# Kernel optimization log

Measured on AMD Instinct MI355X. Metric: run time of the kernel, lower is better.

Reference implementation:

```python
import jax, jax.numpy as jnp
import numpy as np

EPS = 1e-05


def setup_inputs() -> dict:
    key = jax.random.key(0)
    k1, k2, k3, k4 = jax.random.split(key, 4)
    B, N, L, J = 1, 256, 192, 32
    n_feat_out = 128
    d2 = J * J  # 1024
    x_down = jax.random.normal(k1, (B, N, L, J), dtype=jnp.float32)
    x_down_w = jax.random.normal(k2, (B, N, L, J), dtype=jnp.float32)
    a_2 = jnp.ones((d2,), dtype=jnp.float32)
    b_2 = jnp.zeros((d2,), dtype=jnp.float32)
    # nn.Linear default init: U(-1/sqrt(fan_in), 1/sqrt(fan_in))
    bound = 1.0 / np.sqrt(d2)
    W = jax.random.uniform(k3, (d2, n_feat_out), dtype=jnp.float32, minval=-bound, maxval=bound)
    b = jax.random.uniform(k4, (n_feat_out,), dtype=jnp.float32, minval=-bound, maxval=bound)
    return {"x_down": x_down, "x_down_w": x_down_w, "a_2": a_2, "b_2": b_2, "W": W, "b": b}


def reference(x_down, x_down_w, a_2, b_2, W, b):
    B, N, L, J = x_down.shape
    # outer-product contraction over MSA dim: (B,L,L,J,J)
    pair = jnp.einsum('bnij,bnlm->biljm', x_down, x_down_w)
    pair = pair.reshape(B, L, L, J * J)
    # LayerNorm over last dim (biased variance, matching torch unbiased=False)
    mean = pair.mean(axis=-1, keepdims=True)
    var = pair.var(axis=-1, keepdims=True)
    pair = a_2 * (pair - mean) / jnp.sqrt(var + EPS) + b_2
    # Linear projection J^2 -> n_feat_out
    return pair @ W + b
```

## Files before the change

### kernel.cpp

```cpp
#include <hip/hip_runtime.h>
#include <hip/hip_bf16.h>
#include <stdint.h>

#define NN   256
#define LL   192
#define MDIM 6144
#define D2   1024
#define FF   128

typedef __bf16 bf16x8 __attribute__((ext_vector_type(8)));
typedef float  f32x4  __attribute__((ext_vector_type(4)));

#define MFMA16(a, b, c) __builtin_amdgcn_mfma_f32_16x16x32_bf16(a, b, c, 0, 0, 0)

__device__ __forceinline__ void gload_lds16(const void* g, void* l) {
  __builtin_amdgcn_global_load_lds(
      (__attribute__((address_space(1))) void*)(g),
      (__attribute__((address_space(3))) void*)(l),
      16, 0, 0);
}

static __device__ __forceinline__ unsigned short bf16_bits(float v) {
  __bf16 h = (__bf16)v;
  return __builtin_bit_cast(unsigned short, h);
}

__global__ __launch_bounds__(256)
void prep_all(const float* __restrict__ x1, const float* __restrict__ x2,
              const float* __restrict__ W, const float* __restrict__ a2,
              const float* __restrict__ b2, const float* __restrict__ bias,
              __bf16* __restrict__ At, __bf16* __restrict__ Bt,
              __bf16* __restrict__ WB, float* __restrict__ S,
              float* __restrict__ T) {
  __shared__ float tile[32][33];
  const int b = blockIdx.x;
  const int t = threadIdx.x;
  if (b < 3072) {
    const float* src = (b < 1536) ? x1 : x2;
    __bf16* dst = (b < 1536) ? At : Bt;
    const int bb = (b < 1536) ? b : b - 1536;
    const int m0 = (bb % 192) * 32;
    const int k0 = (bb / 192) * 32;
    {
      const int kr = t >> 3, mc = (t & 7) * 4;
      const float4 v = *(const float4*)&src[(size_t)(k0 + kr) * MDIM + m0 + mc];
      tile[kr][mc + 0] = v.x;
      tile[kr][mc + 1] = v.y;
      tile[kr][mc + 2] = v.z;
      tile[kr][mc + 3] = v.w;
    }
    __syncthreads();
    {
      const int mr = t >> 3, kc = (t & 7) * 4;
      ushort4 u;
      u.x = bf16_bits(tile[kc + 0][mr]);
      u.y = bf16_bits(tile[kc + 1][mr]);
      u.z = bf16_bits(tile[kc + 2][mr]);
      u.w = bf16_bits(tile[kc + 3][mr]);
      *(ushort4*)&dst[(size_t)(m0 + mr) * NN + k0 + kc] = u;
    }
  } else {
    const int f = b - 3072;
    float s = 0.f, tt = 0.f;
#pragma unroll
    for (int it = 0; it < 4; ++it) {
      const int k = t + it * 256;
      const float wv = W[(size_t)k * FF + f];
      const __bf16 wa = (__bf16)(a2[k] * wv);
      WB[(size_t)(k >> 5) * 4096 + f * 32 + ((k >> 3) & 3) * 8 + (k & 7)] = wa;
      s += (float)wa;
      tt += b2[k] * wv;
    }
#pragma unroll
    for (int off = 32; off; off >>= 1) {
      s += __shfl_xor(s, off);
      tt += __shfl_xor(tt, off);
    }
    const int wv_ = t >> 6, ln = t & 63;
    if (ln == 0) { tile[0][wv_] = s; tile[1][wv_] = tt; }
    __syncthreads();
    if (t == 0) {
      S[f] = tile[0][0] + tile[0][1] + tile[0][2] + tile[0][3];
      T[f] = tile[1][0] + tile[1][1] + tile[1][2] + tile[1][3] + bias[f];
    }
  }
}

__global__ __launch_bounds__(512, 4)
void fused10(const __bf16* __restrict__ At, const __bf16* __restrict__ Bt,
             const __bf16* __restrict__ WB, const float* __restrict__ S,
             const float* __restrict__ T, float* __restrict__ out) {
  __shared__ uint8_t lds[65536];
  __shared__ float mean_s[32], rstd_s[32];

  const int tid = threadIdx.x;
  const int w = tid >> 6;
  const int lane = tid & 63;
  const int q = lane >> 4;
  const int c = lane & 15;

  const int b = blockIdx.x;
  const int xcd = b & 7;
  const int s_ = b >> 3;
  const int bx = (xcd >> 1) * 12 + (s_ % 12);
  const int by = (xcd & 1) * 12 + (s_ / 12);
  const int m0 = bx * 128, n0 = by * 256;

  uint8_t* As = lds;
  uint8_t* Bs = lds + 16384;

  const int l8 = lane & 7;
  const int r8 = lane >> 3;
  const int gsw = l8 ^ r8;

  f32x4 acc[4][4];
#pragma unroll
  for (int i = 0; i < 4; ++i)
#pragma unroll
    for (int j = 0; j < 4; ++j)
      acc[i][j] = (f32x4){0.f, 0.f, 0.f, 0.f};

  const int mbase = (w & 1) * 64;
  const int nbase = (w >> 1) * 64;

  {
    const __bf16* gA = At + (size_t)(m0 + w * 16 + r8) * NN + gsw * 8;
    const __bf16* gB = Bt + (size_t)(n0 + w * 32 + r8) * NN + gsw * 8;
#pragma unroll 1
    for (int kb = 0; kb < 4; ++kb) {
      __syncthreads();
#pragma unroll
      for (int j = 0; j < 2; ++j)
        gload_lds16(gA + (size_t)j * 8 * NN, As + (w * 16 + j * 8) * 128);
#pragma unroll
      for (int j = 0; j < 4; ++j)
        gload_lds16(gB + (size_t)j * 8 * NN, Bs + (w * 32 + j * 8) * 128);
      __syncthreads();
#pragma unroll
      for (int ks = 0; ks < 2; ++ks) {
        const int slot = ((ks * 4 + q) ^ (lane & 7)) * 16;
        bf16x8 a[4];
#pragma unroll
        for (int t4 = 0; t4 < 4; ++t4)
          a[t4] = *(const bf16x8*)(As + (mbase + t4 * 16 + c) * 128 + slot);
#pragma unroll
        for (int tj = 0; tj < 4; ++tj) {
          const bf16x8 bfr =
              *(const bf16x8*)(Bs + (nbase + tj * 16 + c) * 128 + slot);
#pragma unroll
          for (int ti = 0; ti < 4; ++ti)
            acc[ti][tj] = MFMA16(a[ti], bfr, acc[ti][tj]);
        }
      }
      gA += 64;
      gB += 64;
    }
  }

  const int fs = w * 16;
  const __bf16* wbp = WB + (fs + c) * 32 + q * 8;
  bf16x8 pb[8];
  pb[0] = *(const bf16x8*)(wbp);
  pb[1] = *(const bf16x8*)(wbp + 4096);

  __syncthreads();

  const int i_hi = w & 1, l_hi = w >> 1;
#pragma unroll
  for (int ab = 0; ab < 2; ++ab) {
#pragma unroll
    for (int cb = 0; cb < 2; ++cb) {
      float s1 = 0.f, s2 = 0.f;
#pragma unroll
      for (int dti = 0; dti < 2; ++dti)
#pragma unroll
        for (int dtj = 0; dtj < 2; ++dtj)
#pragma unroll
          for (int reg = 0; reg < 4; ++reg) {
            const float v = acc[ab * 2 + dti][cb * 2 + dtj][reg];
            s1 += v; s2 += v * v;
          }
#pragma unroll
      for (int off = 32; off; off >>= 1) {
        s1 += __shfl_xor(s1, off);
        s2 += __shfl_xor(s2, off);
      }
      const float mean = s1 * (1.0f / 1024.0f);
      const float var = s2 * (1.0f / 1024.0f) - mean * mean;
      const float rstd = rsqrtf(var + 1e-5f);
      const int r = (i_hi * 2 + ab) * 8 + l_hi * 2 + cb;
      if (lane == 0) { mean_s[r] = mean; rstd_s[r] = rstd; }
      const int r7 = r & 7;
#pragma unroll
      for (int dti = 0; dti < 2; ++dti)
#pragma unroll
        for (int dtj = 0; dtj < 2; ++dtj)
#pragma unroll
          for (int rp = 0; rp < 4; rp += 2) {
            const float x = acc[ab * 2 + dti][cb * 2 + dtj][rp];
            const float y = acc[ab * 2 + dti][cb * 2 + dtj][rp + 1];
            const float send = (c & 1) ? x : y;
            const float recv = __shfl_xor(send, 1);
            const float vlo = (c & 1) ? recv : x;
            const float vhi = (c & 1) ? y : recv;
            const int reg_w = (c & 1) ? rp + 1 : rp;
            const int j = dti * 16 + q * 4 + reg_w;
            const int mm0 = dtj * 16 + (c & ~1);
            const int k = j * 32 + mm0;
            const int g = k >> 3;
            const int G = g ^ (g >> 4) ^ r7;
            const uint32_t dw =
                ((uint32_t)bf16_bits(vhi) << 16) | (uint32_t)bf16_bits(vlo);
            *(uint32_t*)(lds + r * 2048 + G * 16 + (mm0 & 7) * 2) = dw;
          }
    }
  }

  __syncthreads();
  __builtin_amdgcn_sched_barrier(0);

#pragma unroll
  for (int p = 2; p < 8; ++p)
    pb[p] = *(const bf16x8*)(wbp + p * 4096);

  f32x4 acc2[2];
  acc2[0] = (f32x4){0.f, 0.f, 0.f, 0.f};
  acc2[1] = (f32x4){0.f, 0.f, 0.f, 0.f};
  const int c7 = c & 7;
#pragma unroll
  for (int kstep = 0; kstep < 32; ++kstep) {
    const int g = kstep * 4 + q;
    const int G = g ^ (g >> 4) ^ c7;
    const bf16x8 a0 = *(const bf16x8*)(lds + c * 2048 + G * 16);
    const bf16x8 a1 = *(const bf16x8*)(lds + (16 + c) * 2048 + G * 16);
    acc2[0] = MFMA16(a0, pb[kstep & 7], acc2[0]);
    acc2[1] = MFMA16(a1, pb[kstep & 7], acc2[1]);
    if (kstep < 24)
      pb[kstep & 7] = *(const bf16x8*)(wbp + (kstep + 8) * 4096);
  }

  const float S0 = S[fs + c], T0 = T[fs + c];
#pragma unroll
  for (int reg = 0; reg < 4; ++reg) {
    const int r0 = q * 4 + reg;
    const int r1 = 16 + r0;
    {
      const float mean = mean_s[r0], rstd = rstd_s[r0];
      const int i = bx * 4 + (r0 >> 3);
      const int l = by * 8 + (r0 & 7);
      out[((size_t)i * LL + l) * FF + fs + c] =
          rstd * (acc2[0][reg] - mean * S0) + T0;
    }
    {
      const float mean = mean_s[r1], rstd = rstd_s[r1];
      const int i = bx * 4 + (r1 >> 3);
      const int l = by * 8 + (r1 & 7);
      out[((size_t)i * LL + l) * FF + fs + c] =
          rstd * (acc2[1][reg] - mean * S0) + T0;
    }
  }
}

extern "C" void kernel_launch(void* const* d_in, const int* in_sizes, int n_in,
                              void* d_out, int out_size, void* d_ws, size_t ws_size,
                              hipStream_t stream) {
  const float* x_down   = (const float*)d_in[0];
  const float* x_down_w = (const float*)d_in[1];
  const float* a2       = (const float*)d_in[2];
  const float* b2       = (const float*)d_in[3];
  const float* W        = (const float*)d_in[4];
  const float* bias     = (const float*)d_in[5];
  float* out = (float*)d_out;

  uint8_t* ws = (uint8_t*)d_ws;
  __bf16* At  = (__bf16*)(ws);
  __bf16* Bt  = (__bf16*)(ws + 3145728);
  __bf16* WB  = (__bf16*)(ws + 6291456);
  float*  S   = (float*)(ws + 6553600);
  float*  T   = (float*)(ws + 6554112);

  prep_all<<<dim3(3200), dim3(256), 0, stream>>>(x_down, x_down_w, W, a2, b2,
                                                 bias, At, Bt, WB, S, T);
  fused10<<<dim3(1152), dim3(512), 0, stream>>>(At, Bt, WB, S, T, out);
}
```

Before: 124.9 us.

## Double-buffer LDS loads and enlarge tiles to 256x256 with 1024-thread blocks

Doubles the M tile per block (256x256 output tile, 16 waves) and double-buffers the A/B LDS tiles so the next K-slice's global-to-LDS loads overlap the current MFMA work, using explicit vmcnt waits. The grid is halved to 576 blocks, with 128 KB of dynamic LDS and the XCD-aware block mapping adjusted to match. Only 8 of the 16 waves run the second projection GEMM, each now handling 64 rows. The large LDS footprint limits residency to one block per CU, and idle waves in the epilogue may reduce utilisation.

```diff
diff --git a/kernel.cpp b/kernel.cpp
--- a/kernel.cpp
+++ b/kernel.cpp
@@ -86,12 +86,12 @@
   }
 }
 
-__global__ __launch_bounds__(512, 4)
-void fused10(const __bf16* __restrict__ At, const __bf16* __restrict__ Bt,
+__global__ __launch_bounds__(1024, 4)
+void fused11(const __bf16* __restrict__ At, const __bf16* __restrict__ Bt,
              const __bf16* __restrict__ WB, const float* __restrict__ S,
              const float* __restrict__ T, float* __restrict__ out) {
-  __shared__ uint8_t lds[65536];
-  __shared__ float mean_s[32], rstd_s[32];
+  extern __shared__ uint8_t lds[];
+  __shared__ float mean_s[64], rstd_s[64];
 
   const int tid = threadIdx.x;
   const int w = tid >> 6;
@@ -102,12 +102,14 @@
   const int b = blockIdx.x;
   const int xcd = b & 7;
   const int s_ = b >> 3;
-  const int bx = (xcd >> 1) * 12 + (s_ % 12);
-  const int by = (xcd & 1) * 12 + (s_ / 12);
-  const int m0 = bx * 128, n0 = by * 256;
-
-  uint8_t* As = lds;
-  uint8_t* Bs = lds + 16384;
+  const int bx = (xcd >> 1) * 6 + (s_ % 6);
+  const int by = (xcd & 1) * 12 + (s_ / 6);
+  const int m0 = bx * 256, n0 = by * 256;
+
+  uint8_t* As0 = lds;
+  uint8_t* Bs0 = lds + 32768;
+  uint8_t* As1 = lds + 65536;
+  uint8_t* Bs1 = lds + 98304;
 
   const int l8 = lane & 7;
   const int r8 = lane >> 3;
@@ -120,52 +122,69 @@
     for (int j = 0; j < 4; ++j)
       acc[i][j] = (f32x4){0.f, 0.f, 0.f, 0.f};
 
-  const int mbase = (w & 1) * 64;
-  const int nbase = (w >> 1) * 64;
-
-  {
-    const __bf16* gA = At + (size_t)(m0 + w * 16 + r8) * NN + gsw * 8;
-    const __bf16* gB = Bt + (size_t)(n0 + w * 32 + r8) * NN + gsw * 8;
-#pragma unroll 1
-    for (int kb = 0; kb < 4; ++kb) {
-      __syncthreads();
+  const int mbase = (w & 3) * 64;
+  const int nbase = (w >> 2) * 64;
+
+  const __bf16* gA = At + (size_t)(m0 + w * 16 + r8) * NN + gsw * 8;
+  const __bf16* gB = Bt + (size_t)(n0 + w * 16 + r8) * NN + gsw * 8;
+
+#pragma unroll
+  for (int j = 0; j < 2; ++j)
+    gload_lds16(gA + (size_t)j * 8 * NN, As0 + (w * 16 + j * 8) * 128);
+#pragma unroll
+  for (int j = 0; j < 2; ++j)
+    gload_lds16(gB + (size_t)j * 8 * NN, Bs0 + (w * 16 + j * 8) * 128);
+
+#pragma unroll
+  for (int kb = 0; kb < 4; ++kb) {
+    uint8_t* Ac = (kb & 1) ? As1 : As0;
+    uint8_t* Bc = (kb & 1) ? Bs1 : Bs0;
+    if (kb < 3) {
+      uint8_t* An = (kb & 1) ? As0 : As1;
+      uint8_t* Bn = (kb & 1) ? Bs0 : Bs1;
+      const __bf16* ga = gA + (size_t)(kb + 1) * 64;
+      const __bf16* gb = gB + (size_t)(kb + 1) * 64;
 #pragma unroll
       for (int j = 0; j < 2; ++j)
-        gload_lds16(gA + (size_t)j * 8 * NN, As + (w * 16 + j * 8) * 128);
-#pragma unroll
-      for (int j = 0; j < 4; ++j)
-        gload_lds16(gB + (size_t)j * 8 * NN, Bs + (w * 32 + j * 8) * 128);
-      __syncthreads();
-#pragma unroll
-      for (int ks = 0; ks < 2; ++ks) {
-        const int slot = ((ks * 4 + q) ^ (lane & 7)) * 16;
-        bf16x8 a[4];
-#pragma unroll
-        for (int t4 = 0; t4 < 4; ++t4)
-          a[t4] = *(const bf16x8*)(As + (mbase + t4 * 16 + c) * 128 + slot);
-#pragma unroll
-        for (int tj = 0; tj < 4; ++tj) {
-          const bf16x8 bfr =
-              *(const bf16x8*)(Bs + (nbase + tj * 16 + c) * 128 + slot);
-#pragma unroll
-          for (int ti = 0; ti < 4; ++ti)
-            acc[ti][tj] = MFMA16(a[ti], bfr, acc[ti][tj]);
-        }
+        gload_lds16(ga + (size_t)j * 8 * NN, An + (w * 16 + j * 8) * 128);
+#pragma unroll
+      for (int j = 0; j < 2; ++j)
+        gload_lds16(gb + (size_t)j * 8 * NN, Bn + (w * 16 + j * 8) * 128);
+      asm volatile("s_waitcnt vmcnt(4)" ::: "memory");
+    } else {
+      asm volatile("s_waitcnt vmcnt(0)" ::: "memory");
+    }
+    __builtin_amdgcn_s_barrier();
+    __builtin_amdgcn_sched_barrier(0);
+#pragma unroll
+    for (int ks = 0; ks < 2; ++ks) {
+      const int slot = ((ks * 4 + q) ^ l8) * 16;
+      bf16x8 a[4];
+#pragma unroll
+      for (int t4 = 0; t4 < 4; ++t4)
+        a[t4] = *(const bf16x8*)(Ac + (mbase + t4 * 16 + c) * 128 + slot);
+#pragma unroll
+      for (int tj = 0; tj < 4; ++tj) {
+        const bf16x8 bfr =
+            *(const bf16x8*)(Bc + (nbase + tj * 16 + c) * 128 + slot);
+#pragma unroll
+        for (int ti = 0; ti < 4; ++ti)
+          acc[ti][tj] = MFMA16(a[ti], bfr, acc[ti][tj]);
       }
-      gA += 64;
-      gB += 64;
-    }
+    }
+    asm volatile("s_waitcnt lgkmcnt(0)" ::: "memory");
+    __builtin_amdgcn_s_barrier();
   }
 
   const int fs = w * 16;
   const __bf16* wbp = WB + (fs + c) * 32 + q * 8;
   bf16x8 pb[8];
-  pb[0] = *(const bf16x8*)(wbp);
-  pb[1] = *(const bf16x8*)(wbp + 4096);
-
-  __syncthreads();
-
-  const int i_hi = w & 1, l_hi = w >> 1;
+  if (w < 8) {
+    pb[0] = *(const bf16x8*)(wbp);
+    pb[1] = *(const bf16x8*)(wbp + 4096);
+  }
+
+  const int i_hi = w & 3, l_hi = w >> 2;
 #pragma unroll
   for (int ab = 0; ab < 2; ++ab) {
 #pragma unroll
@@ -217,47 +236,45 @@
   }
 
   __syncthreads();
-  __builtin_amdgcn_sched_barrier(0);
-
-#pragma unroll
-  for (int p = 2; p < 8; ++p)
-    pb[p] = *(const bf16x8*)(wbp + p * 4096);
-
-  f32x4 acc2[2];
-  acc2[0] = (f32x4){0.f, 0.f, 0.f, 0.f};
-  acc2[1] = (f32x4){0.f, 0.f, 0.f, 0.f};
-  const int c7 = c & 7;
-#pragma unroll
-  for (int kstep = 0; kstep < 32; ++kstep) {
-    const int g = kstep * 4 + q;
-    const int G = g ^ (g >> 4) ^ c7;
-    const bf16x8 a0 = *(const bf16x8*)(lds + c * 2048 + G * 16);
-    const bf16x8 a1 = *(const bf16x8*)(lds + (16 + c) * 2048 + G * 16);
-    acc2[0] = MFMA16(a0, pb[kstep & 7], acc2[0]);
-    acc2[1] = MFMA16(a1, pb[kstep & 7], acc2[1]);
-    if (kstep < 24)
-      pb[kstep & 7] = *(const bf16x8*)(wbp + (kstep + 8) * 4096);
-  }
-
-  const float S0 = S[fs + c], T0 = T[fs + c];
-#pragma unroll
-  for (int reg = 0; reg < 4; ++reg) {
-    const int r0 = q * 4 + reg;
-    const int r1 = 16 + r0;
-    {
-      const float mean = mean_s[r0], rstd = rstd_s[r0];
-      const int i = bx * 4 + (r0 >> 3);
-      const int l = by * 8 + (r0 & 7);
-      out[((size_t)i * LL + l) * FF + fs + c] =
-          rstd * (acc2[0][reg] - mean * S0) + T0;
-    }
-    {
-      const float mean = mean_s[r1], rstd = rstd_s[r1];
-      const int i = bx * 4 + (r1 >> 3);
-      const int l = by * 8 + (r1 & 7);
-      out[((size_t)i * LL + l) * FF + fs + c] =
-          rstd * (acc2[1][reg] - mean * S0) + T0;
-    }
+
+  if (w < 8) {
+    __builtin_amdgcn_sched_barrier(0);
+#pragma unroll
+    for (int p = 2; p < 8; ++p)
+      pb[p] = *(const bf16x8*)(wbp + p * 4096);
+
+    f32x4 acc2[4];
+#pragma unroll
+    for (int rr = 0; rr < 4; ++rr) acc2[rr] = (f32x4){0.f, 0.f, 0.f, 0.f};
+    const int c7 = c & 7;
+#pragma unroll
+    for (int kstep = 0; kstep < 32; ++kstep) {
+      const int g = kstep * 4 + q;
+      const int G = g ^ (g >> 4) ^ c7;
+      const bf16x8 a0 = *(const bf16x8*)(lds + (size_t)(c)      * 2048 + G * 16);
+      const bf16x8 a1 = *(const bf16x8*)(lds + (size_t)(16 + c) * 2048 + G * 16);
+      const bf16x8 a2 = *(const bf16x8*)(lds + (size_t)(32 + c) * 2048 + G * 16);
+      const bf16x8 a3 = *(const bf16x8*)(lds + (size_t)(48 + c) * 2048 + G * 16);
+      acc2[0] = MFMA16(a0, pb[kstep & 7], acc2[0]);
+      acc2[1] = MFMA16(a1, pb[kstep & 7], acc2[1]);
+      acc2[2] = MFMA16(a2, pb[kstep & 7], acc2[2]);
+      acc2[3] = MFMA16(a3, pb[kstep & 7], acc2[3]);
+      if (kstep < 24)
+        pb[kstep & 7] = *(const bf16x8*)(wbp + (kstep + 8) * 4096);
+    }
+
+    const float S0 = S[fs + c], T0 = T[fs + c];
+#pragma unroll
+    for (int rr = 0; rr < 4; ++rr)
+#pragma unroll
+      for (int reg = 0; reg < 4; ++reg) {
+        const int r = rr * 16 + q * 4 + reg;
+        const float mean = mean_s[r], rstd = rstd_s[r];
+        const int i = bx * 8 + (r >> 3);
+        const int l = by * 8 + (r & 7);
+        out[((size_t)i * LL + l) * FF + fs + c] =
+            rstd * (acc2[rr][reg] - mean * S0) + T0;
+      }
   }
 }
 
@@ -279,7 +296,10 @@
   float*  S   = (float*)(ws + 6553600);
   float*  T   = (float*)(ws + 6554112);
 
+  hipFuncSetAttribute((const void*)fused11,
+                      hipFuncAttributeMaxDynamicSharedMemorySize, 131072);
+
   prep_all<<<dim3(3200), dim3(256), 0, stream>>>(x_down, x_down_w, W, a2, b2,
                                                  bias, At, Bt, WB, S, T);
-  fused10<<<dim3(1152), dim3(512), 0, stream>>>(At, Bt, WB, S, T, out);
-}
+  fused11<<<dim3(576), dim3(1024), 131072, stream>>>(At, Bt, WB, S, T, out);
+}
```

New measurement: 128.6 us. +3.0%, slower.

## Double-buffer LDS K-tiles with async global loads to overlap GEMM loads and MFMA

Applied to the files above, without the earlier changes.

Replaces the single-buffered 64-wide K loop (4 iterations, two full syncthreads each) with a double-buffered 32-wide K loop (8 iterations). The next tile is prefetched into the alternate LDS buffer via global_load_lds, with explicit vmcnt waits and raw s_barrier. The swizzle is adapted to the narrower 64-byte rows. The aim is to hide global-to-LDS latency behind MFMA work, at the cost of more barriers per K and a finer-grained pipeline.

```diff
diff --git a/kernel.cpp b/kernel.cpp
--- a/kernel.cpp
+++ b/kernel.cpp
@@ -87,7 +87,7 @@
 }
 
 __global__ __launch_bounds__(512, 4)
-void fused10(const __bf16* __restrict__ At, const __bf16* __restrict__ Bt,
+void fused12(const __bf16* __restrict__ At, const __bf16* __restrict__ Bt,
              const __bf16* __restrict__ WB, const float* __restrict__ S,
              const float* __restrict__ T, float* __restrict__ out) {
   __shared__ uint8_t lds[65536];
@@ -106,12 +106,13 @@
   const int by = (xcd & 1) * 12 + (s_ / 12);
   const int m0 = bx * 128, n0 = by * 256;
 
-  uint8_t* As = lds;
-  uint8_t* Bs = lds + 16384;
-
-  const int l8 = lane & 7;
-  const int r8 = lane >> 3;
-  const int gsw = l8 ^ r8;
+  uint8_t* As0 = lds;
+  uint8_t* As1 = lds + 8192;
+  uint8_t* Bs0 = lds + 16384;
+  uint8_t* Bs1 = lds + 32768;
+
+  const int r16 = lane >> 2;
+  const int ksw = (lane & 3) ^ (r16 & 3);
 
   f32x4 acc[4][4];
 #pragma unroll
@@ -123,38 +124,48 @@
   const int mbase = (w & 1) * 64;
   const int nbase = (w >> 1) * 64;
 
-  {
-    const __bf16* gA = At + (size_t)(m0 + w * 16 + r8) * NN + gsw * 8;
-    const __bf16* gB = Bt + (size_t)(n0 + w * 32 + r8) * NN + gsw * 8;
-#pragma unroll 1
-    for (int kb = 0; kb < 4; ++kb) {
-      __syncthreads();
-#pragma unroll
-      for (int j = 0; j < 2; ++j)
-        gload_lds16(gA + (size_t)j * 8 * NN, As + (w * 16 + j * 8) * 128);
-#pragma unroll
-      for (int j = 0; j < 4; ++j)
-        gload_lds16(gB + (size_t)j * 8 * NN, Bs + (w * 32 + j * 8) * 128);
-      __syncthreads();
-#pragma unroll
-      for (int ks = 0; ks < 2; ++ks) {
-        const int slot = ((ks * 4 + q) ^ (lane & 7)) * 16;
-        bf16x8 a[4];
-#pragma unroll
-        for (int t4 = 0; t4 < 4; ++t4)
-          a[t4] = *(const bf16x8*)(As + (mbase + t4 * 16 + c) * 128 + slot);
-#pragma unroll
-        for (int tj = 0; tj < 4; ++tj) {
-          const bf16x8 bfr =
-              *(const bf16x8*)(Bs + (nbase + tj * 16 + c) * 128 + slot);
-#pragma unroll
-          for (int ti = 0; ti < 4; ++ti)
-            acc[ti][tj] = MFMA16(a[ti], bfr, acc[ti][tj]);
-        }
+  const __bf16* gA = At + (size_t)(m0 + w * 16 + r16) * NN + ksw * 8;
+  const __bf16* gB = Bt + (size_t)(n0 + w * 32 + r16) * NN + ksw * 8;
+
+  gload_lds16(gA, As0 + w * 1024);
+  gload_lds16(gB, Bs0 + w * 2048);
+  gload_lds16(gB + (size_t)16 * NN, Bs0 + w * 2048 + 1024);
+
+#pragma unroll
+  for (int kb = 0; kb < 8; ++kb) {
+    uint8_t* Ac = (kb & 1) ? As1 : As0;
+    uint8_t* Bc = (kb & 1) ? Bs1 : Bs0;
+    if (kb < 7) {
+      uint8_t* An = (kb & 1) ? As0 : As1;
+      uint8_t* Bn = (kb & 1) ? Bs0 : Bs1;
+      const __bf16* ga = gA + (size_t)(kb + 1) * 32;
+      const __bf16* gb = gB + (size_t)(kb + 1) * 32;
+      gload_lds16(ga, An + w * 1024);
+      gload_lds16(gb, Bn + w * 2048);
+      gload_lds16(gb + (size_t)16 * NN, Bn + w * 2048 + 1024);
+      asm volatile("s_waitcnt vmcnt(3)" ::: "memory");
+    } else {
+      asm volatile("s_waitcnt vmcnt(0)" ::: "memory");
+    }
+    __builtin_amdgcn_s_barrier();
+    __builtin_amdgcn_sched_barrier(0);
+    {
+      const int slot = (q ^ (c & 3)) * 16;
+      bf16x8 a[4];
+#pragma unroll
+      for (int t4 = 0; t4 < 4; ++t4)
+        a[t4] = *(const bf16x8*)(Ac + (mbase + t4 * 16 + c) * 64 + slot);
+#pragma unroll
+      for (int tj = 0; tj < 4; ++tj) {
+        const bf16x8 bfr =
+            *(const bf16x8*)(Bc + (nbase + tj * 16 + c) * 64 + slot);
+#pragma unroll
+        for (int ti = 0; ti < 4; ++ti)
+          acc[ti][tj] = MFMA16(a[ti], bfr, acc[ti][tj]);
       }
-      gA += 64;
-      gB += 64;
-    }
+    }
+    asm volatile("s_waitcnt lgkmcnt(0)" ::: "memory");
+    __builtin_amdgcn_s_barrier();
   }
 
   const int fs = w * 16;
@@ -163,7 +174,6 @@
   pb[0] = *(const bf16x8*)(wbp);
   pb[1] = *(const bf16x8*)(wbp + 4096);
 
-  __syncthreads();
 
   const int i_hi = w & 1, l_hi = w >> 1;
 #pragma unroll
@@ -281,5 +291,5 @@
 
   prep_all<<<dim3(3200), dim3(256), 0, stream>>>(x_down, x_down_w, W, a2, b2,
                                                  bias, At, Bt, WB, S, T);
-  fused10<<<dim3(1152), dim3(512), 0, stream>>>(At, Bt, WB, S, T, out);
-}
+  fused12<<<dim3(1152), dim3(512), 0, stream>>>(At, Bt, WB, S, T, out);
+}
```

Result: slower. 129.7 us (+3.9%).
